# Optimization experiments

Hardware: AMD Instinct MI355X
Metric: run time of the kernel (lower is better)

Reference implementation:

```python
import jax, jax.numpy as jnp
import numpy as np

D = 2048        # dim
H = 16          # n_heads
FFN = 4 * D     # ffn hidden
K = 8192        # working-memory slots
HID = 32        # halt-gate hidden
EPS = 1e-5      # LayerNorm eps


def setup_inputs() -> dict:
    key = jax.random.key(0)
    ks = jax.random.split(key, 16)
    s = 0.02  # weight init scale for numerical sanity
    def rn(k, shape, scale=s):
        return jax.random.normal(k, shape, dtype=jnp.float32) * scale
    return {
        "workspace": jax.random.normal(ks[0], (D,), dtype=jnp.float32),
        "wm_context": jax.random.normal(ks[1], (K, D), dtype=jnp.float32),
        "self_in_w": rn(ks[2], (3 * D, D)), "self_in_b": jnp.zeros((3 * D,), jnp.float32),
        "self_out_w": rn(ks[3], (D, D)), "self_out_b": jnp.zeros((D,), jnp.float32),
        "cross_in_w": rn(ks[4], (3 * D, D)), "cross_in_b": jnp.zeros((3 * D,), jnp.float32),
        "cross_out_w": rn(ks[5], (D, D)), "cross_out_b": jnp.zeros((D,), jnp.float32),
        "ffn_w1": rn(ks[6], (FFN, D)), "ffn_b1": jnp.zeros((FFN,), jnp.float32),
        "ffn_w2": rn(ks[7], (D, FFN)), "ffn_b2": jnp.zeros((D,), jnp.float32),
        "ln1_g": jnp.ones((D,), jnp.float32), "ln1_b": jnp.zeros((D,), jnp.float32),
        "ln2_g": jnp.ones((D,), jnp.float32), "ln2_b": jnp.zeros((D,), jnp.float32),
        "ln3_g": jnp.ones((D,), jnp.float32), "ln3_b": jnp.zeros((D,), jnp.float32),
        "halt_w1": rn(ks[8], (HID, D)), "halt_b1": jnp.zeros((HID,), jnp.float32),
        "halt_w2": rn(ks[9], (1, HID)), "halt_b2": jnp.zeros((1,), jnp.float32),
        "max_steps": 5,
    }


def _ln(x, g, b):
    m = x.mean()
    v = jnp.mean((x - m) ** 2)
    return (x - m) / jnp.sqrt(v + EPS) * g + b


def _mha(xq, xkv, in_w, in_b, out_w, out_b):
    # xq: (D,) single query token; xkv: (L, D) keys/values. Eval mode (no dropout).
    d = xq.shape[-1]
    hd = d // H
    wq, wk, wv = in_w[:d], in_w[d:2 * d], in_w[2 * d:]
    bq, bk, bv = in_b[:d], in_b[d:2 * d], in_b[2 * d:]
    q = (xq @ wq.T + bq).reshape(H, hd)            # (H, hd)
    k = (xkv @ wk.T + bk).reshape(-1, H, hd)       # (L, H, hd)
    v = (xkv @ wv.T + bv).reshape(-1, H, hd)       # (L, H, hd)
    scores = jnp.einsum("hd,khd->hk", q, k) * (hd ** -0.5)  # (H, L)
    attn = jax.nn.softmax(scores, axis=-1)
    o = jnp.einsum("hk,khd->hd", attn, v).reshape(d)
    return o @ out_w.T + out_b


def reference(workspace, wm_context,
              self_in_w, self_in_b, self_out_w, self_out_b,
              cross_in_w, cross_in_b, cross_out_w, cross_out_b,
              ffn_w1, ffn_b1, ffn_w2, ffn_b2,
              ln1_g, ln1_b, ln2_g, ln2_b, ln3_g, ln3_b,
              halt_w1, halt_b1, halt_w2, halt_b2, max_steps):
    state = workspace
    cum = jnp.float32(0.0)
    acc = jnp.zeros_like(state)
    active = jnp.bool_(True)
    for _ in range(max_steps):  # fixed small loop over ACT steps
        cross = _mha(state, wm_context, cross_in_w, cross_in_b, cross_out_w, cross_out_b)
        s1 = _ln(state + cross, ln1_g, ln1_b)
        sa = _mha(s1, s1[None, :], self_in_w, self_in_b, self_out_w, self_out_b)
        s2 = _ln(s1 + sa, ln2_g, ln2_b)
        h = jax.nn.gelu(s2 @ ffn_w1.T + ffn_b1, approximate=False)
        new_state = _ln(s2 + (h @ ffn_w2.T + ffn_b2), ln3_g, ln3_b)
        hh = jax.nn.gelu(new_state @ halt_w1.T + halt_b1, approximate=False)
        halt = jax.nn.sigmoid(hh @ halt_w2.T + halt_b2)[0]
        new_cum = cum + halt
        halts = new_cum >= 1.0 - 1e-6
        # remainder = 1 - cum_before if halting, else halt_prob
        w = jnp.where(halts, 1.0 - cum, halt)
        acc = acc + jnp.where(active, w, 0.0) * new_state
        state = jnp.where(active, new_state, state)
        cum = jnp.where(active, new_cum, cum)
        active = jnp.logical_and(active, jnp.logical_not(halts))
    # if loop exhausted without halting, add leftover mass on last state
    acc = acc + jnp.where(cum < 1.0 - 1e-6, 1.0 - cum, 0.0) * state
    return acc
```

## Files before the change

kernel.cpp:

```cpp
#include <hip/hip_runtime.h>
#include <math.h>

#define DD 2048
#define NH 16
#define HDIM 128
#define NK 8192
#define NFFN 8192
#define NHID 32
#define EPSV 1e-5f

typedef __attribute__((ext_vector_type(8))) short bf16x8;
typedef __attribute__((ext_vector_type(4))) float f32x4;

static const size_t W_ST  = 0;
static const size_t W_AC  = 2048;
static const size_t W_SC  = 4096;
static const size_t W_Q   = 4160;
static const size_t W_T   = 6208;
static const size_t W_TB  = 38976;
static const size_t W_PS  = 55360;
static const size_t W_P   = 1103936;
static const size_t W_PB  = 1235008;
static const size_t W_U   = 1300544;
static const size_t W_O   = 1333312;
static const size_t W_CR  = 1335360;
static const size_t W_S1  = 1337408;
static const size_t W_V   = 1339456;
static const size_t W_SA  = 1341504;
static const size_t W_S2  = 1343552;
static const size_t W_H1  = 1345600;
static const size_t W_F2  = 1353792;
static const size_t W_NS  = 1355840;
static const size_t W_PUA = 1357888;
static const size_t W_PUB = 1882176;
static const size_t W_WMB = 1882176;
static const size_t W_WMT = 10270784;
static const size_t W_ENDA  = 18659392;
static const size_t W_ENDB  = 6076480;

__device__ __forceinline__ float gelu_exact(float x) {
  return 0.5f * x * (1.0f + erff(x * 0.70710678118654752f));
}
__device__ __forceinline__ unsigned short f2bf(float x) {
  unsigned u = __float_as_uint(x);
  u += 0x7FFFu + ((u >> 16) & 1u);
  return (unsigned short)(u >> 16);
}

__device__ __forceinline__ float wave_dot(const float* __restrict__ w, const float* x, int C) {
  int lane = threadIdx.x & 63;
  float acc = 0.f;
  for (int c = lane * 4; c < C; c += 256) {
    float4 wv = *reinterpret_cast<const float4*>(w + c);
    float4 xx = *reinterpret_cast<const float4*>(x + c);
    acc += wv.x * xx.x + wv.y * xx.y + wv.z * xx.z + wv.w * xx.w;
  }
#pragma unroll
  for (int off = 32; off; off >>= 1) acc += __shfl_xor(acc, off, 64);
  return acc;
}

__device__ void block_ln(const float* x1, const float* x2,
                         const float* __restrict__ g, const float* __restrict__ be,
                         float* o, float* red) {
  int tid = threadIdx.x;
  float loc[8]; float s = 0.f;
#pragma unroll
  for (int j = 0; j < 8; ++j) { int i = tid * 8 + j; float v = x1[i] + x2[i]; loc[j] = v; s += v; }
#pragma unroll
  for (int off = 32; off; off >>= 1) s += __shfl_xor(s, off, 64);
  __syncthreads();
  if ((tid & 63) == 0) red[tid >> 6] = s;
  __syncthreads();
  float m = (red[0] + red[1] + red[2] + red[3]) * (1.f / 2048.f);
  s = 0.f;
#pragma unroll
  for (int j = 0; j < 8; ++j) { float d = loc[j] - m; s += d * d; }
#pragma unroll
  for (int off = 32; off; off >>= 1) s += __shfl_xor(s, off, 64);
  __syncthreads();
  if ((tid & 63) == 0) red[tid >> 6] = s;
  __syncthreads();
  float inv = 1.f / sqrtf((red[0] + red[1] + red[2] + red[3]) * (1.f / 2048.f) + EPSV);
#pragma unroll
  for (int j = 0; j < 8; ++j) { int i = tid * 8 + j; o[i] = (loc[j] - m) * inv * g[i] + be[i]; }
  __syncthreads();
}

__global__ void init_kernel(const float* __restrict__ w0, float* __restrict__ state,
                            float* __restrict__ acc, float* __restrict__ scal) {
  int i = blockIdx.x * 256 + threadIdx.x;
  if (i < DD) { state[i] = w0[i]; acc[i] = 0.f; }
  if (i == 0) { scal[0] = 0.f; scal[1] = 1.f; }
}

__global__ void prep_wm(const float* __restrict__ wm, unsigned short* __restrict__ wmb,
                        unsigned short* __restrict__ wmbT) {
  __shared__ unsigned short tile[64][72];
  int bk = blockIdx.x & 127, bc = blockIdx.x >> 7;
  int k0 = bk * 64, c0 = bc * 64;
  int tx = threadIdx.x & 15, ty = threadIdx.x >> 4;
#pragma unroll
  for (int rr = 0; rr < 4; ++rr) {
    int r = ty + rr * 16;
    float4 v = *reinterpret_cast<const float4*>(wm + (size_t)(k0 + r) * DD + c0 + tx * 4);
    ushort4 u4;
    u4.x = f2bf(v.x); u4.y = f2bf(v.y); u4.z = f2bf(v.z); u4.w = f2bf(v.w);
    *reinterpret_cast<ushort4*>(wmb + (size_t)(k0 + r) * DD + c0 + tx * 4) = u4;
    tile[tx * 4 + 0][r] = u4.x; tile[tx * 4 + 1][r] = u4.y;
    tile[tx * 4 + 2][r] = u4.z; tile[tx * 4 + 3][r] = u4.w;
  }
  __syncthreads();
#pragma unroll
  for (int rr = 0; rr < 4; ++rr) {
    int c = ty + rr * 16;
    ushort4 o;
    o.x = tile[c][tx * 4]; o.y = tile[c][tx * 4 + 1];
    o.z = tile[c][tx * 4 + 2]; o.w = tile[c][tx * 4 + 3];
    *reinterpret_cast<ushort4*>(wmbT + (size_t)(c0 + c) * NK + k0 + tx * 4) = o;
  }
}

__global__ void matvec_kernel(const float* __restrict__ W, const float* __restrict__ bias,
                              const float* __restrict__ x, float* __restrict__ y,
                              int R, int C, int act, int perhead,
                              const float* __restrict__ scal, int gated) {
  if (gated && scal[1] == 0.f) return;
  int wid = threadIdx.x >> 6, lane = threadIdx.x & 63;
  int row = blockIdx.x * 4 + wid;
  if (row >= R) return;
  const float* w = W + (size_t)row * C;
  const float* xv = perhead ? (x + (size_t)(row >> 7) * C) : x;
  float acc = 0.f;
  for (int c = lane * 4; c < C; c += 256) {
    float4 wv = *reinterpret_cast<const float4*>(w + c);
    float4 xx = *reinterpret_cast<const float4*>(xv + c);
    acc += wv.x * xx.x + wv.y * xx.y + wv.z * xx.z + wv.w * xx.w;
  }
  for (int off = 32; off > 0; off >>= 1) acc += __shfl_xor(acc, off, 64);
  if (lane == 0) {
    float r = acc + bias[row];
    if (act == 1) r = gelu_exact(r);
    y[row] = r;
  }
}

__global__ void tproj_kernel(const float* __restrict__ Wk, const float* __restrict__ q,
                             float* __restrict__ t, unsigned short* __restrict__ tb,
                             int obf, const float* __restrict__ scal) {
  if (scal[1] == 0.f) return;
  int h = blockIdx.x >> 4, ct = blockIdx.x & 15;
  int c = ct * 128 + threadIdx.x;
  const float* wb = Wk + (size_t)(h * HDIM) * DD + c;
  const float* qh = q + h * HDIM;
  float acc = 0.f;
  for (int d = 0; d < HDIM; ++d) acc += qh[d] * wb[(size_t)d * DD];
  if (obf) tb[h * DD + c] = f2bf(acc);
  else     t[h * DD + c] = acc;
}

__global__ __launch_bounds__(256, 4) void scores_mfma(const unsigned short* __restrict__ wmb,
                                                      const unsigned short* __restrict__ tb,
                                                      float* __restrict__ part_s,
                                                      const float* __restrict__ scal) {
  if (scal[1] == 0.f) return;
  int w = threadIdx.x >> 6, lane = threadIdx.x & 63;
  int task = blockIdx.x * 4 + w;
  int cc = task & 7, rg = task >> 3;
  int r0 = rg * 16, c0 = cc * 256;
  int l15 = lane & 15, kg = lane >> 4;
  const unsigned short* ap = wmb + (size_t)(r0 + l15) * DD + c0 + kg * 8;
  const unsigned short* bp = tb + (size_t)l15 * DD + c0 + kg * 8;
  bf16x8 a[8], b[8];
#pragma unroll
  for (int i = 0; i < 8; ++i) {
    a[i] = *reinterpret_cast<const bf16x8*>(ap + i * 32);
    b[i] = *reinterpret_cast<const bf16x8*>(bp + i * 32);
  }
  f32x4 acc = {0.f, 0.f, 0.f, 0.f};
#pragma unroll
  for (int i = 0; i < 8; ++i)
    acc = __builtin_amdgcn_mfma_f32_16x16x32_bf16(a[i], b[i], acc, 0, 0, 0);
  float* op = part_s + ((size_t)cc * NH + l15) * NK + r0 + kg * 4;
#pragma unroll
  for (int r = 0; r < 4; ++r) op[r] = acc[r];
}

__global__ __launch_bounds__(256, 4) void u_mfma(const unsigned short* __restrict__ wmbT,
                                                 const unsigned short* __restrict__ pb,
                                                 float* __restrict__ part_u,
                                                 const float* __restrict__ scal) {
  if (scal[1] == 0.f) return;
  int w = threadIdx.x >> 6, lane = threadIdx.x & 63;
  int task = blockIdx.x * 4 + w;
  int ct = task & 127, kc = task >> 7;
  int c0 = ct * 16, k0 = kc * 512;
  int l15 = lane & 15, kg = lane >> 4;
  const unsigned short* ap = pb + (size_t)l15 * NK + k0 + kg * 8;
  const unsigned short* bp = wmbT + (size_t)(c0 + l15) * NK + k0 + kg * 8;
  f32x4 acc = {0.f, 0.f, 0.f, 0.f};
#pragma unroll
  for (int half = 0; half < 2; ++half) {
    bf16x8 a[8], b[8];
#pragma unroll
    for (int i = 0; i < 8; ++i) {
      a[i] = *reinterpret_cast<const bf16x8*>(ap + half * 256 + i * 32);
      b[i] = *reinterpret_cast<const bf16x8*>(bp + half * 256 + i * 32);
    }
#pragma unroll
    for (int i = 0; i < 8; ++i)
      acc = __builtin_amdgcn_mfma_f32_16x16x32_bf16(a[i], b[i], acc, 0, 0, 0);
  }
  float* op = part_u + ((size_t)kc * NH + kg * 4) * DD + c0 + l15;
#pragma unroll
  for (int r = 0; r < 4; ++r) op[(size_t)r * DD] = acc[r];
}

__global__ void softmax_kernel(const float* __restrict__ part_s, float* __restrict__ p,
                               unsigned short* __restrict__ pb, int obf,
                               const float* __restrict__ scal) {
  if (scal[1] == 0.f) return;
  int h = blockIdx.x, tid = threadIdx.x;
  __shared__ float red[256];
  float v[32]; float mx = -1e30f;
  for (int j = 0; j < 32; ++j) {
    int k = tid + j * 256; float s = 0.f;
    for (int cc = 0; cc < 8; ++cc) s += part_s[((size_t)cc * NH + h) * NK + k];
    s *= 0.08838834764831845f;
    v[j] = s; mx = fmaxf(mx, s);
  }
  red[tid] = mx; __syncthreads();
  for (int off = 128; off > 0; off >>= 1) { if (tid < off) red[tid] = fmaxf(red[tid], red[tid + off]); __syncthreads(); }
  mx = red[0]; __syncthreads();
  float sum = 0.f;
  for (int j = 0; j < 32; ++j) { v[j] = expf(v[j] - mx); sum += v[j]; }
  red[tid] = sum; __syncthreads();
  for (int off = 128; off > 0; off >>= 1) { if (tid < off) red[tid] += red[tid + off]; __syncthreads(); }
  float inv = 1.f / red[0];
  for (int j = 0; j < 32; ++j) {
    float val = v[j] * inv;
    size_t idx = (size_t)h * NK + tid + j * 256;
    if (obf) pb[idx] = f2bf(val);
    else     p[idx] = val;
  }
}

__global__ __launch_bounds__(256) void o_fused_kernel(const float* __restrict__ part_u,
                                                      const float* __restrict__ Wv,
                                                      const float* __restrict__ bv,
                                                      float* __restrict__ O,
                                                      const float* __restrict__ scal) {
  if (scal[1] == 0.f) return;
  __shared__ float uh[2048];
  int tid = threadIdx.x, wid = tid >> 6, lane = tid & 63;
  int h = blockIdx.x >> 5;
#pragma unroll
  for (int j = 0; j < 8; ++j) {
    int c = tid + j * 256;
    float ss = 0.f;
#pragma unroll
    for (int kc = 0; kc < 16; ++kc) ss += part_u[((size_t)kc * NH + h) * DD + c];
    uh[c] = ss;
  }
  __syncthreads();
  int row = h * HDIM + (blockIdx.x & 31) * 4 + wid;
  float a = wave_dot(Wv + (size_t)row * DD, uh, DD);
  if (lane == 0) O[row] = a + bv[row];
}

__global__ __launch_bounds__(256) void v_ln1_kernel(const float* __restrict__ ST,
                                                    const float* __restrict__ CR,
                                                    const float* __restrict__ g1,
                                                    const float* __restrict__ b1,
                                                    const float* __restrict__ W,
                                                    const float* __restrict__ bias,
                                                    float* __restrict__ V,
                                                    const float* __restrict__ scal) {
  if (scal[1] == 0.f) return;
  __shared__ float s1[2048];
  __shared__ float red[8];
  block_ln(ST, CR, g1, b1, s1, red);
  int wid = threadIdx.x >> 6, lane = threadIdx.x & 63;
  int row = blockIdx.x * 4 + wid;
  float a = wave_dot(W + (size_t)row * DD, s1, DD);
  if (lane == 0) V[row] = a + bias[row];
}

__global__ __launch_bounds__(256) void ffn1_kernel(const float* __restrict__ ST,
                                                   const float* __restrict__ CR,
                                                   const float* __restrict__ SA,
                                                   const float* __restrict__ g1,
                                                   const float* __restrict__ b1,
                                                   const float* __restrict__ g2,
                                                   const float* __restrict__ b2,
                                                   const float* __restrict__ W,
                                                   const float* __restrict__ bias,
                                                   float* __restrict__ H1,
                                                   const float* __restrict__ scal) {
  if (scal[1] == 0.f) return;
  __shared__ float s1[2048];
  __shared__ float s2[2048];
  __shared__ float red[8];
  block_ln(ST, CR, g1, b1, s1, red);
  block_ln(s1, SA, g2, b2, s2, red);
  int wid = threadIdx.x >> 6, lane = threadIdx.x & 63;
  int gw = blockIdx.x * 4 + wid;
  for (int r = gw; r < NFFN; r += 2048) {
    float a = wave_dot(W + (size_t)r * DD, s2, DD);
    if (lane == 0) H1[r] = gelu_exact(a + bias[r]);
  }
}

__global__ void act_ln3_kernel(const float* __restrict__ ST, const float* __restrict__ CR,
                               const float* __restrict__ SA, const float* __restrict__ F2,
                               const float* __restrict__ g1, const float* __restrict__ b1,
                               const float* __restrict__ g2, const float* __restrict__ b2,
                               const float* __restrict__ g3, const float* __restrict__ b3,
                               const float* __restrict__ hw1, const float* __restrict__ hb1,
                               const float* __restrict__ hw2, const float* __restrict__ hb2,
                               float* __restrict__ state, float* __restrict__ acc,
                               float* __restrict__ scal, const int* __restrict__ max_steps,
                               int step) {
  if (step >= max_steps[0]) return;
  if (scal[1] == 0.f) return;
  __shared__ float sA[2048];
  __shared__ float sB[2048];
  __shared__ float red[8];
  __shared__ float hh[NHID];
  __shared__ float wbc;
  int tid = threadIdx.x;
  block_ln(ST, CR, g1, b1, sA, red);
  block_ln(sA, SA, g2, b2, sB, red);
  block_ln(sB, F2, g3, b3, sA, red);
  int row = tid >> 3, seg = tid & 7;
  const float* wr = hw1 + (size_t)row * DD + seg * 256;
  const float* np = sA + seg * 256;
  float s = 0.f;
  for (int i = 0; i < 256; ++i) s += wr[i] * np[i];
  sB[row * 8 + seg] = s;
  __syncthreads();
  if (tid < NHID) {
    float t2 = hb1[tid];
#pragma unroll
    for (int j = 0; j < 8; ++j) t2 += sB[tid * 8 + j];
    hh[tid] = gelu_exact(t2);
  }
  __syncthreads();
  if (tid == 0) {
    float hs = hb2[0];
    for (int j = 0; j < NHID; ++j) hs += hh[j] * hw2[j];
    float halt = 1.f / (1.f + expf(-hs));
    float cum = scal[0];
    float ncum = cum + halt;
    int halts = (ncum >= 1.f - 1e-6f);
    wbc = halts ? (1.f - cum) : halt;
    scal[0] = ncum;
    scal[1] = halts ? 0.f : 1.f;
  }
  __syncthreads();
  float w = wbc;
  for (int i = tid; i < DD; i += 256) { acc[i] += w * sA[i]; state[i] = sA[i]; }
}

__global__ void final_kernel(const float* __restrict__ state, const float* __restrict__ acc,
                             const float* __restrict__ scal, float* __restrict__ out) {
  float cum = scal[0];
  float w = (cum < 1.f - 1e-6f) ? (1.f - cum) : 0.f;
  int i = blockIdx.x * 256 + threadIdx.x;
  if (i < DD) out[i] = acc[i] + w * state[i];
}


#define FMA16(wvv, tp)                                                       \
  {                                                                          \
    float4 t0 = tp[0], t1 = tp[1], t2 = tp[2], t3 = tp[3];                   \
    acc[0] += wvv * t0.x; acc[1] += wvv * t0.y;                              \
    acc[2] += wvv * t0.z; acc[3] += wvv * t0.w;                              \
    acc[4] += wvv * t1.x; acc[5] += wvv * t1.y;                              \
    acc[6] += wvv * t1.z; acc[7] += wvv * t1.w;                              \
    acc[8] += wvv * t2.x; acc[9] += wvv * t2.y;                              \
    acc[10] += wvv * t2.z; acc[11] += wvv * t2.w;                            \
    acc[12] += wvv * t3.x; acc[13] += wvv * t3.y;                            \
    acc[14] += wvv * t3.z; acc[15] += wvv * t3.w;                            \
  }

__global__ void scores_kernel(const float* __restrict__ wm, const float* __restrict__ t,
                              float* __restrict__ part_s, const float* __restrict__ scal) {
  if (scal[1] == 0.f) return;
  int kt = blockIdx.x >> 3, cc = blockIdx.x & 7;
  int tid = threadIdx.x;
  int k0 = kt * 128, c0 = cc * 256;
  __shared__ float wlds[128 * 33];
  __shared__ float tlds[256 * 20];
  for (int j = 0; j < 32; ++j) {
    int idx = j * 128 + tid;
    int h = idx >> 8, c = idx & 255;
    tlds[c * 20 + h] = t[(size_t)h * DD + c0 + c];
  }
  float acc[NH];
#pragma unroll
  for (int h = 0; h < NH; ++h) acc[h] = 0.f;
  for (int sl = 0; sl < 8; ++sl) {
    int cbase = c0 + sl * 32;
    __syncthreads();
    for (int p = 0; p < 8; ++p) {
      int f = p * 128 + tid;
      int r = f >> 3, fc = f & 7;
      float4 v = *reinterpret_cast<const float4*>(wm + (size_t)(k0 + r) * DD + cbase + fc * 4);
      float* d = wlds + r * 33 + fc * 4;
      d[0] = v.x; d[1] = v.y; d[2] = v.z; d[3] = v.w;
    }
    __syncthreads();
    const float* myrow = wlds + tid * 33;
#pragma unroll 4
    for (int cb = 0; cb < 32; ++cb) {
      float wvv = myrow[cb];
      const float4* tp = reinterpret_cast<const float4*>(tlds + (size_t)(sl * 32 + cb) * 20);
      FMA16(wvv, tp);
    }
  }
#pragma unroll
  for (int h = 0; h < NH; ++h)
    part_s[((size_t)cc * NH + h) * NK + k0 + tid] = acc[h];
}

#define U1FMA(i, ph) \
  acc[i].x += w4.x * (ph); acc[i].y += w4.y * (ph); \
  acc[i].z += w4.z * (ph); acc[i].w += w4.w * (ph);

template <int KCH>
__global__ void u1_kernel(const float* __restrict__ wm, const float* __restrict__ p,
                          float* __restrict__ part_u, const float* __restrict__ scal) {
  if (scal[1] == 0.f) return;
  int kc = blockIdx.x >> 2, ct = blockIdx.x & 3;
  int tid = threadIdx.x;
  int k0 = kc * KCH;
  int c = ct * 512 + tid * 4;
  __shared__ float plds[KCH * 16];
  for (int j = 0; j < KCH * 16 / 128; ++j) {
    int idx = j * 128 + tid;
    int h = idx / KCH, k = idx % KCH;
    plds[k * 16 + h] = p[(size_t)h * NK + k0 + k];
  }
  __syncthreads();
  float4 acc[NH];
#pragma unroll
  for (int h = 0; h < NH; ++h) acc[h] = make_float4(0.f, 0.f, 0.f, 0.f);
#pragma unroll 2
  for (int k = 0; k < KCH; ++k) {
    float4 w4 = *reinterpret_cast<const float4*>(wm + (size_t)(k0 + k) * DD + c);
    const float4* pp = reinterpret_cast<const float4*>(plds + k * 16);
    float4 p0 = pp[0], p1 = pp[1], p2 = pp[2], p3 = pp[3];
    U1FMA(0, p0.x)  U1FMA(1, p0.y)  U1FMA(2, p0.z)  U1FMA(3, p0.w)
    U1FMA(4, p1.x)  U1FMA(5, p1.y)  U1FMA(6, p1.z)  U1FMA(7, p1.w)
    U1FMA(8, p2.x)  U1FMA(9, p2.y)  U1FMA(10, p2.z) U1FMA(11, p2.w)
    U1FMA(12, p3.x) U1FMA(13, p3.y) U1FMA(14, p3.z) U1FMA(15, p3.w)
  }
#pragma unroll
  for (int h = 0; h < NH; ++h)
    *reinterpret_cast<float4*>(part_u + ((size_t)kc * NH + h) * DD + c) = acc[h];
}

__global__ void u2_kernel(const float* __restrict__ part_u, float* __restrict__ u,
                          const float* __restrict__ scal, int nkc) {
  if (scal[1] == 0.f) return;
  int i = blockIdx.x * 256 + threadIdx.x;
  float s = 0.f;
  for (int kc = 0; kc < nkc; ++kc) s += part_u[(size_t)kc * NH * DD + i];
  u[i] = s;
}

__global__ void ln_kernel(const float* __restrict__ a, const float* __restrict__ r,
                          const float* __restrict__ g, const float* __restrict__ beta,
                          float* __restrict__ out, const float* __restrict__ scal) {
  if (scal[1] == 0.f) return;
  __shared__ float red[256];
  __shared__ float mv[2];
  int tid = threadIdx.x;
  float x[8]; float s = 0.f;
  for (int j = 0; j < 8; ++j) { int i = tid * 8 + j; x[j] = a[i] + r[i]; s += x[j]; }
  red[tid] = s; __syncthreads();
  for (int off = 128; off > 0; off >>= 1) { if (tid < off) red[tid] += red[tid + off]; __syncthreads(); }
  if (tid == 0) mv[0] = red[0] * (1.f / DD);
  __syncthreads();
  float m = mv[0]; s = 0.f;
  for (int j = 0; j < 8; ++j) { float d = x[j] - m; s += d * d; }
  red[tid] = s; __syncthreads();
  for (int off = 128; off > 0; off >>= 1) { if (tid < off) red[tid] += red[tid + off]; __syncthreads(); }
  if (tid == 0) mv[1] = 1.f / sqrtf(red[0] * (1.f / DD) + EPSV);
  __syncthreads();
  float inv = mv[1];
  for (int j = 0; j < 8; ++j) { int i = tid * 8 + j; out[i] = (x[j] - m) * inv * g[i] + beta[i]; }
}

__global__ void act_kernel(const float* __restrict__ hw1, const float* __restrict__ hb1,
                           const float* __restrict__ hw2, const float* __restrict__ hb2,
                           const float* __restrict__ ns, float* __restrict__ state,
                           float* __restrict__ acc, float* __restrict__ scal,
                           const int* __restrict__ max_steps, int step) {
  if (step >= max_steps[0]) return;
  if (scal[1] == 0.f) return;
  __shared__ float red[NHID][9];
  __shared__ float hh[NHID];
  __shared__ float wbc;
  int tid = threadIdx.x;
  int row = tid >> 3, seg = tid & 7;
  const float* wr = hw1 + (size_t)row * DD + seg * 256;
  const float* nsp = ns + seg * 256;
  float s = 0.f;
  for (int i = 0; i < 256; ++i) s += wr[i] * nsp[i];
  red[row][seg] = s; __syncthreads();
  if (tid < NHID) {
    float t = hb1[tid];
    for (int j = 0; j < 8; ++j) t += red[tid][j];
    hh[tid] = gelu_exact(t);
  }
  __syncthreads();
  if (tid == 0) {
    float hs = hb2[0];
    for (int j = 0; j < NHID; ++j) hs += hh[j] * hw2[j];
    float halt = 1.f / (1.f + expf(-hs));
    float cum = scal[0];
    float ncum = cum + halt;
    int halts = (ncum >= 1.f - 1e-6f);
    wbc = halts ? (1.f - cum) : halt;
    scal[0] = ncum;
    scal[1] = halts ? 0.f : 1.f;
  }
  __syncthreads();
  float w = wbc;
  for (int i = tid; i < DD; i += 256) { acc[i] += w * ns[i]; state[i] = ns[i]; }
}

extern "C" void kernel_launch(void* const* d_in, const int* in_sizes, int n_in,
                              void* d_out, int out_size, void* d_ws, size_t ws_size,
                              hipStream_t stream) {
  const float* workspace   = (const float*)d_in[0];
  const float* wm          = (const float*)d_in[1];
  const float* self_in_w   = (const float*)d_in[2];
  const float* self_in_b   = (const float*)d_in[3];
  const float* self_out_w  = (const float*)d_in[4];
  const float* self_out_b  = (const float*)d_in[5];
  const float* cross_in_w  = (const float*)d_in[6];
  const float* cross_in_b  = (const float*)d_in[7];
  const float* cross_out_w = (const float*)d_in[8];
  const float* cross_out_b = (const float*)d_in[9];
  const float* ffn_w1      = (const float*)d_in[10];
  const float* ffn_b1      = (const float*)d_in[11];
  const float* ffn_w2      = (const float*)d_in[12];
  const float* ffn_b2      = (const float*)d_in[13];
  const float* ln1_g = (const float*)d_in[14];
  const float* ln1_b = (const float*)d_in[15];
  const float* ln2_g = (const float*)d_in[16];
  const float* ln2_b = (const float*)d_in[17];
  const float* ln3_g = (const float*)d_in[18];
  const float* ln3_b = (const float*)d_in[19];
  const float* halt_w1 = (const float*)d_in[20];
  const float* halt_b1 = (const float*)d_in[21];
  const float* halt_w2 = (const float*)d_in[22];
  const float* halt_b2 = (const float*)d_in[23];
  const int*   max_steps = (const int*)d_in[24];

  float* ws = (float*)d_ws;
  float* out = (float*)d_out;

  float* ST = ws + W_ST;  float* AC = ws + W_AC;  float* SC = ws + W_SC;
  float* Q_ = ws + W_Q;   float* PS = ws + W_PS;  float* O_ = ws + W_O;
  float* CR = ws + W_CR;  float* V_ = ws + W_V;   float* SA = ws + W_SA;
  float* H1 = ws + W_H1;  float* F2 = ws + W_F2;  float* PU = ws + W_PUA;
  unsigned short* TB  = (unsigned short*)(ws + W_TB);
  unsigned short* PB  = (unsigned short*)(ws + W_PB);
  unsigned short* WMB = (unsigned short*)(ws + W_WMB);
  unsigned short* WMT = (unsigned short*)(ws + W_WMT);

  const bool tierA = W_ENDA * sizeof(float) <= ws_size;

  init_kernel<<<8, 256, 0, stream>>>(workspace, ST, AC, SC);

  if (tierA) {
    prep_wm<<<4096, 256, 0, stream>>>(wm, WMB, WMT);
    for (int s = 0; s < 5; ++s) {
      matvec_kernel<<<512, 256, 0, stream>>>(cross_in_w, cross_in_b, ST, Q_, DD, DD, 0, 0, SC, 1);
      tproj_kernel<<<256, 128, 0, stream>>>(cross_in_w + (size_t)DD * DD, Q_, nullptr, TB, 1, SC);
      scores_mfma<<<1024, 256, 0, stream>>>(WMB, TB, PS, SC);
      softmax_kernel<<<16, 256, 0, stream>>>(PS, nullptr, PB, 1, SC);
      u_mfma<<<512, 256, 0, stream>>>(WMT, PB, PU, SC);
      o_fused_kernel<<<512, 256, 0, stream>>>(PU, cross_in_w + (size_t)2 * DD * DD,
                                              cross_in_b + 2 * DD, O_, SC);
      matvec_kernel<<<512, 256, 0, stream>>>(cross_out_w, cross_out_b, O_, CR, DD, DD, 0, 0, SC, 1);
      v_ln1_kernel<<<512, 256, 0, stream>>>(ST, CR, ln1_g, ln1_b,
                                            self_in_w + (size_t)2 * DD * DD,
                                            self_in_b + 2 * DD, V_, SC);
      matvec_kernel<<<512, 256, 0, stream>>>(self_out_w, self_out_b, V_, SA, DD, DD, 0, 0, SC, 1);
      ffn1_kernel<<<512, 256, 0, stream>>>(ST, CR, SA, ln1_g, ln1_b, ln2_g, ln2_b,
                                           ffn_w1, ffn_b1, H1, SC);
      matvec_kernel<<<512, 256, 0, stream>>>(ffn_w2, ffn_b2, H1, F2, DD, NFFN, 0, 0, SC, 1);
      act_ln3_kernel<<<1, 256, 0, stream>>>(ST, CR, SA, F2, ln1_g, ln1_b, ln2_g, ln2_b,
                                            ln3_g, ln3_b, halt_w1, halt_b1, halt_w2, halt_b2,
                                            ST, AC, SC, max_steps, s);
    }
  } else {
    float* T_ = ws + W_T;   float* P_ = ws + W_P;   float* U_ = ws + W_U;
    float* S1 = ws + W_S1;  float* S2 = ws + W_S2;  float* NS = ws + W_NS;
    float* PUB = ws + W_PUB;
    const bool bigB = W_ENDB * sizeof(float) <= ws_size;
    for (int s = 0; s < 5; ++s) {
      matvec_kernel<<<512, 256, 0, stream>>>(cross_in_w, cross_in_b, ST, Q_, DD, DD, 0, 0, SC, 1);
      tproj_kernel<<<256, 128, 0, stream>>>(cross_in_w + (size_t)DD * DD, Q_, T_, nullptr, 0, SC);
      scores_kernel<<<512, 128, 0, stream>>>(wm, T_, PS, SC);
      softmax_kernel<<<16, 256, 0, stream>>>(PS, P_, nullptr, 0, SC);
      if (bigB) u1_kernel<64><<<512, 128, 0, stream>>>(wm, P_, PUB, SC);
      else      u1_kernel<256><<<128, 128, 0, stream>>>(wm, P_, PUB, SC);
      u2_kernel<<<128, 256, 0, stream>>>(PUB, U_, SC, bigB ? 128 : 32);
      matvec_kernel<<<512, 256, 0, stream>>>(cross_in_w + (size_t)2 * DD * DD, cross_in_b + 2 * DD,
                                             U_, O_, DD, DD, 0, 1, SC, 1);
      matvec_kernel<<<512, 256, 0, stream>>>(cross_out_w, cross_out_b, O_, CR, DD, DD, 0, 0, SC, 1);
      ln_kernel<<<1, 256, 0, stream>>>(ST, CR, ln1_g, ln1_b, S1, SC);
      matvec_kernel<<<512, 256, 0, stream>>>(self_in_w + (size_t)2 * DD * DD, self_in_b + 2 * DD,
                                             S1, V_, DD, DD, 0, 0, SC, 1);
      matvec_kernel<<<512, 256, 0, stream>>>(self_out_w, self_out_b, V_, SA, DD, DD, 0, 0, SC, 1);
      ln_kernel<<<1, 256, 0, stream>>>(S1, SA, ln2_g, ln2_b, S2, SC);
      matvec_kernel<<<2048, 256, 0, stream>>>(ffn_w1, ffn_b1, S2, H1, NFFN, DD, 1, 0, SC, 1);
      matvec_kernel<<<512, 256, 0, stream>>>(ffn_w2, ffn_b2, H1, F2, DD, NFFN, 0, 0, SC, 1);
      ln_kernel<<<1, 256, 0, stream>>>(S2, F2, ln3_g, ln3_b, NS, SC);
      act_kernel<<<1, 256, 0, stream>>>(halt_w1, halt_b1, halt_w2, halt_b2, NS, ST, AC, SC,
                                        max_steps, s);
    }
  }
  final_kernel<<<8, 256, 0, stream>>>(ST, AC, SC, out);
}
```

Before: 368.1 us.

## Run last two ACT steps as cooperative persistent kernels with grid syncs

```diff
diff --git a/kernel.cpp b/kernel.cpp
--- a/kernel.cpp
+++ b/kernel.cpp
@@ -1,5 +1,8 @@
 #include <hip/hip_runtime.h>
+#include <hip/hip_cooperative_groups.h>
 #include <math.h>
+
+namespace cg = cooperative_groups;
 
 #define DD 2048
 #define NH 16
@@ -95,7 +98,13 @@
 }
 
 __global__ void prep_wm(const float* __restrict__ wm, unsigned short* __restrict__ wmb,
-                        unsigned short* __restrict__ wmbT) {
+                        unsigned short* __restrict__ wmbT,
+                        const float* __restrict__ w0, float* __restrict__ state,
+                        float* __restrict__ acc, float* __restrict__ scal) {
+  if (blockIdx.x == 0) {
+    for (int i = threadIdx.x; i < DD; i += 256) { state[i] = w0[i]; acc[i] = 0.f; }
+    if (threadIdx.x == 0) { scal[0] = 0.f; scal[1] = 1.f; }
+  }
   __shared__ unsigned short tile[64][72];
   int bk = blockIdx.x & 127, bc = blockIdx.x >> 7;
   int k0 = bk * 64, c0 = bc * 64;
@@ -368,6 +377,190 @@
   float w = (cum < 1.f - 1e-6f) ? (1.f - cum) : 0.f;
   int i = blockIdx.x * 256 + threadIdx.x;
   if (i < DD) out[i] = acc[i] + w * state[i];
+}
+
+struct MegaP {
+  const float *self_in_w, *self_in_b, *self_out_w, *self_out_b;
+  const float *cross_in_w, *cross_in_b, *cross_out_w, *cross_out_b;
+  const float *ffn_w1, *ffn_b1, *ffn_w2, *ffn_b2;
+  const float *ln1_g, *ln1_b, *ln2_g, *ln2_b, *ln3_g, *ln3_b;
+  const float *hw1, *hb1, *hw2, *hb2;
+  const int* max_steps;
+  const unsigned short *wmb, *wmt;
+  float *ST, *AC, *SC, *Q;
+  unsigned short *TB, *PB;
+  float *PS, *PU, *O, *CR, *V, *SA, *H1, *F2;
+  int step;
+};
+
+__global__ __launch_bounds__(256, 4) void mega_step(MegaP P) {
+  if (P.step >= P.max_steps[0]) return;
+  if (P.SC[1] == 0.f) return;
+  cg::grid_group grd = cg::this_grid();
+  __shared__ float sxA[2048];
+  __shared__ float sxB[2048];
+  __shared__ float red[8];
+  const int tid = threadIdx.x, bid = blockIdx.x, nb = gridDim.x;
+  const int wid = tid >> 6, lane = tid & 63;
+  const int gw = bid * 4 + wid, nw = nb * 4;
+  const int l15 = lane & 15, kg = lane >> 4;
+
+  for (int r = gw; r < DD; r += nw) {
+    float a = wave_dot(P.cross_in_w + (size_t)r * DD, P.ST, DD);
+    if (lane == 0) P.Q[r] = a + P.cross_in_b[r];
+  }
+  grd.sync();
+  for (int idx = bid * 256 + tid; idx < NH * DD; idx += nb * 256) {
+    int h = idx >> 11, c = idx & 2047;
+    const float* wb = P.cross_in_w + (size_t)DD * DD + (size_t)(h * HDIM) * DD + c;
+    const float* qh = P.Q + h * HDIM;
+    float acc = 0.f;
+    for (int d = 0; d < HDIM; ++d) acc += qh[d] * wb[(size_t)d * DD];
+    P.TB[idx] = f2bf(acc);
+  }
+  grd.sync();
+  for (int task = gw; task < 4096; task += nw) {
+    int cc = task & 7, rg = task >> 3;
+    int r0 = rg * 16, c0 = cc * 256;
+    const unsigned short* ap = P.wmb + (size_t)(r0 + l15) * DD + c0 + kg * 8;
+    const unsigned short* bp = P.TB + (size_t)l15 * DD + c0 + kg * 8;
+    f32x4 acc = {0.f, 0.f, 0.f, 0.f};
+#pragma unroll
+    for (int q4 = 0; q4 < 2; ++q4) {
+      bf16x8 a[4], b[4];
+#pragma unroll
+      for (int i = 0; i < 4; ++i) {
+        a[i] = *reinterpret_cast<const bf16x8*>(ap + q4 * 128 + i * 32);
+        b[i] = *reinterpret_cast<const bf16x8*>(bp + q4 * 128 + i * 32);
+      }
+#pragma unroll
+      for (int i = 0; i < 4; ++i)
+        acc = __builtin_amdgcn_mfma_f32_16x16x32_bf16(a[i], b[i], acc, 0, 0, 0);
+    }
+    float* op = P.PS + ((size_t)cc * NH + l15) * NK + r0 + kg * 4;
+#pragma unroll
+    for (int r = 0; r < 4; ++r) op[r] = acc[r];
+  }
+  grd.sync();
+  for (int h = bid; h < NH; h += nb) {
+    float v[32]; float mx = -1e30f;
+    for (int j = 0; j < 32; ++j) {
+      int k = tid + j * 256; float ss = 0.f;
+      for (int cc = 0; cc < 8; ++cc) ss += P.PS[((size_t)cc * NH + h) * NK + k];
+      ss *= 0.08838834764831845f; v[j] = ss; mx = fmaxf(mx, ss);
+    }
+    sxA[tid] = mx; __syncthreads();
+    for (int off = 128; off; off >>= 1) { if (tid < off) sxA[tid] = fmaxf(sxA[tid], sxA[tid + off]); __syncthreads(); }
+    mx = sxA[0]; __syncthreads();
+    float sum = 0.f;
+    for (int j = 0; j < 32; ++j) { v[j] = expf(v[j] - mx); sum += v[j]; }
+    sxA[tid] = sum; __syncthreads();
+    for (int off = 128; off; off >>= 1) { if (tid < off) sxA[tid] += sxA[tid + off]; __syncthreads(); }
+    float inv = 1.f / sxA[0]; __syncthreads();
+    for (int j = 0; j < 32; ++j) P.PB[(size_t)h * NK + tid + j * 256] = f2bf(v[j] * inv);
+  }
+  grd.sync();
+  for (int task = gw; task < 2048; task += nw) {
+    int ct = task & 127, kc = task >> 7;
+    int c0 = ct * 16, k0 = kc * 512;
+    const unsigned short* ap = P.PB + (size_t)l15 * NK + k0 + kg * 8;
+    const unsigned short* bp = P.wmt + (size_t)(c0 + l15) * NK + k0 + kg * 8;
+    f32x4 acc = {0.f, 0.f, 0.f, 0.f};
+#pragma unroll
+    for (int q4 = 0; q4 < 4; ++q4) {
+      bf16x8 a[4], b[4];
+#pragma unroll
+      for (int i = 0; i < 4; ++i) {
+        a[i] = *reinterpret_cast<const bf16x8*>(ap + q4 * 128 + i * 32);
+        b[i] = *reinterpret_cast<const bf16x8*>(bp + q4 * 128 + i * 32);
+      }
+#pragma unroll
+      for (int i = 0; i < 4; ++i)
+        acc = __builtin_amdgcn_mfma_f32_16x16x32_bf16(a[i], b[i], acc, 0, 0, 0);
+    }
+    float* op = P.PU + ((size_t)kc * NH + kg * 4) * DD + c0 + l15;
+#pragma unroll
+    for (int r = 0; r < 4; ++r) op[(size_t)r * DD] = acc[r];
+  }
+  grd.sync();
+  for (int task = bid; task < 512; task += nb) {
+    int h = task >> 5;
+#pragma unroll 2
+    for (int j = 0; j < 8; ++j) {
+      int c = tid * 8 + j;
+      float ss = 0.f;
+#pragma unroll
+      for (int kc = 0; kc < 16; ++kc) ss += P.PU[((size_t)kc * NH + h) * DD + c];
+      sxA[c] = ss;
+    }
+    __syncthreads();
+    int row = h * HDIM + (task & 31) * 4 + wid;
+    float a = wave_dot(P.cross_in_w + (size_t)2 * DD * DD + (size_t)row * DD, sxA, DD);
+    if (lane == 0) P.O[row] = a + P.cross_in_b[2 * DD + row];
+    __syncthreads();
+  }
+  grd.sync();
+  for (int r = gw; r < DD; r += nw) {
+    float a = wave_dot(P.cross_out_w + (size_t)r * DD, P.O, DD);
+    if (lane == 0) P.CR[r] = a + P.cross_out_b[r];
+  }
+  grd.sync();
+  block_ln(P.ST, P.CR, P.ln1_g, P.ln1_b, sxA, red);
+  for (int r = gw; r < DD; r += nw) {
+    float a = wave_dot(P.self_in_w + (size_t)2 * DD * DD + (size_t)r * DD, sxA, DD);
+    if (lane == 0) P.V[r] = a + P.self_in_b[2 * DD + r];
+  }
+  grd.sync();
+  for (int r = gw; r < DD; r += nw) {
+    float a = wave_dot(P.self_out_w + (size_t)r * DD, P.V, DD);
+    if (lane == 0) P.SA[r] = a + P.self_out_b[r];
+  }
+  grd.sync();
+  block_ln(P.ST, P.CR, P.ln1_g, P.ln1_b, sxA, red);
+  block_ln(sxA, P.SA, P.ln2_g, P.ln2_b, sxB, red);
+  for (int r = gw; r < NFFN; r += nw) {
+    float a = wave_dot(P.ffn_w1 + (size_t)r * DD, sxB, DD);
+    if (lane == 0) P.H1[r] = gelu_exact(a + P.ffn_b1[r]);
+  }
+  grd.sync();
+  for (int r = gw; r < DD; r += nw) {
+    float a = wave_dot(P.ffn_w2 + (size_t)r * NFFN, P.H1, NFFN);
+    if (lane == 0) P.F2[r] = a + P.ffn_b2[r];
+  }
+  grd.sync();
+  if (bid == 0) {
+    block_ln(P.ST, P.CR, P.ln1_g, P.ln1_b, sxA, red);
+    block_ln(sxA, P.SA, P.ln2_g, P.ln2_b, sxB, red);
+    block_ln(sxB, P.F2, P.ln3_g, P.ln3_b, sxA, red);
+    int row = tid >> 3, seg = tid & 7;
+    const float* wr = P.hw1 + (size_t)row * DD + seg * 256;
+    const float* np = sxA + seg * 256;
+    float ss = 0.f;
+    for (int i = 0; i < 256; ++i) ss += wr[i] * np[i];
+    sxB[row * 8 + seg] = ss;
+    __syncthreads();
+    if (tid < NHID) {
+      float t2 = P.hb1[tid];
+#pragma unroll
+      for (int j = 0; j < 8; ++j) t2 += sxB[tid * 8 + j];
+      sxB[256 + tid] = gelu_exact(t2);
+    }
+    __syncthreads();
+    if (tid == 0) {
+      float hs = P.hb2[0];
+      for (int j = 0; j < NHID; ++j) hs += sxB[256 + j] * P.hw2[j];
+      float halt = 1.f / (1.f + expf(-hs));
+      float cum = P.SC[0];
+      float ncum = cum + halt;
+      int halts = (ncum >= 1.f - 1e-6f);
+      sxB[300] = halts ? (1.f - cum) : halt;
+      P.SC[0] = ncum;
+      P.SC[1] = halts ? 0.f : 1.f;
+    }
+    __syncthreads();
+    float wv2 = sxB[300];
+    for (int i = tid; i < DD; i += 256) { P.AC[i] += wv2 * sxA[i]; P.ST[i] = sxA[i]; }
+  }
 }
 
 
@@ -575,11 +768,10 @@
 
   const bool tierA = W_ENDA * sizeof(float) <= ws_size;
 
-  init_kernel<<<8, 256, 0, stream>>>(workspace, ST, AC, SC);
-
   if (tierA) {
-    prep_wm<<<4096, 256, 0, stream>>>(wm, WMB, WMT);
-    for (int s = 0; s < 5; ++s) {
+    prep_wm<<<4096, 256, 0, stream>>>(wm, WMB, WMT, workspace, ST, AC, SC);
+
+    for (int s = 0; s < 3; ++s) {
       matvec_kernel<<<512, 256, 0, stream>>>(cross_in_w, cross_in_b, ST, Q_, DD, DD, 0, 0, SC, 1);
       tproj_kernel<<<256, 128, 0, stream>>>(cross_in_w + (size_t)DD * DD, Q_, nullptr, TB, 1, SC);
       scores_mfma<<<1024, 256, 0, stream>>>(WMB, TB, PS, SC);
@@ -599,11 +791,35 @@
                                             ln3_g, ln3_b, halt_w1, halt_b1, halt_w2, halt_b2,
                                             ST, AC, SC, max_steps, s);
     }
+
+    MegaP p;
+    p.self_in_w = self_in_w;   p.self_in_b = self_in_b;
+    p.self_out_w = self_out_w; p.self_out_b = self_out_b;
+    p.cross_in_w = cross_in_w; p.cross_in_b = cross_in_b;
+    p.cross_out_w = cross_out_w; p.cross_out_b = cross_out_b;
+    p.ffn_w1 = ffn_w1; p.ffn_b1 = ffn_b1; p.ffn_w2 = ffn_w2; p.ffn_b2 = ffn_b2;
+    p.ln1_g = ln1_g; p.ln1_b = ln1_b; p.ln2_g = ln2_g; p.ln2_b = ln2_b;
+    p.ln3_g = ln3_g; p.ln3_b = ln3_b;
+    p.hw1 = halt_w1; p.hb1 = halt_b1; p.hw2 = halt_w2; p.hb2 = halt_b2;
+    p.max_steps = max_steps;
+    p.wmb = WMB; p.wmt = WMT;
+    p.ST = ST; p.AC = AC; p.SC = SC; p.Q = Q_;
+    p.TB = TB; p.PB = PB;
+    p.PS = PS; p.PU = PU; p.O = O_; p.CR = CR;
+    p.V = V_; p.SA = SA; p.H1 = H1; p.F2 = F2;
+
+    MegaP p3 = p; p3.step = 3;
+    MegaP p4 = p; p4.step = 4;
+    void* a3[] = {(void*)&p3};
+    void* a4[] = {(void*)&p4};
+    hipLaunchCooperativeKernel((const void*)mega_step, dim3(512), dim3(256), a3, 0, stream);
+    hipLaunchCooperativeKernel((const void*)mega_step, dim3(512), dim3(256), a4, 0, stream);
   } else {
     float* T_ = ws + W_T;   float* P_ = ws + W_P;   float* U_ = ws + W_U;
     float* S1 = ws + W_S1;  float* S2 = ws + W_S2;  float* NS = ws + W_NS;
     float* PUB = ws + W_PUB;
     const bool bigB = W_ENDB * sizeof(float) <= ws_size;
+    init_kernel<<<8, 256, 0, stream>>>(workspace, ST, AC, SC);
     for (int s = 0; s < 5; ++s) {
       matvec_kernel<<<512, 256, 0, stream>>>(cross_in_w, cross_in_b, ST, Q_, DD, DD, 0, 0, SC, 1);
       tproj_kernel<<<256, 128, 0, stream>>>(cross_in_w + (size_t)DD * DD, Q_, T_, nullptr, 0, SC);
```

Measured after the change: 397.7 us. 8.0% more time.
